# Kernel tuning notes

Hardware: AMD Instinct MI355X
Metric: run time of the kernel (lower is better)

Reference implementation:

```python
import jax, jax.numpy as jnp
import numpy as np

LSTM_DIM = 512
SENT_LEN = 384  # n words -> n+2 LSTM positions (START/STOP)


def _lstm_scan(xs, Wih, Whh, b):
    """Unidirectional LSTM over xs [T, D] -> hidden states [T, H]. torch gate order i,f,g,o."""
    H = Whh.shape[1]
    gx = xs @ Wih.T + b  # [T, 4H] precompute input contribution

    def step(carry, g_x):
        h, c = carry
        g = g_x + h @ Whh.T
        i, f, gg, o = jnp.split(g, 4)
        i = jax.nn.sigmoid(i); f = jax.nn.sigmoid(f); o = jax.nn.sigmoid(o)
        c = f * c + i * jnp.tanh(gg)
        h = o * jnp.tanh(c)
        return (h, c), h

    init = (jnp.zeros((H,), xs.dtype), jnp.zeros((H,), xs.dtype))
    _, hs = jax.lax.scan(step, init, gx)
    return hs  # [T, H]


def setup_inputs() -> dict:
    key = jax.random.key(0)
    ks = jax.random.split(key, 16)
    T = SENT_LEN + 2
    H = LSTM_DIM
    s = lambda fan: 1.0 / np.sqrt(fan)
    return {
        "tag_ids": jax.random.randint(ks[0], (T,), 0, 50, dtype=jnp.int32),
        "word_ids": jax.random.randint(ks[1], (T,), 0, 10000, dtype=jnp.int32),
        "tag_emb": jax.random.normal(ks[2], (50, 128), jnp.float32) * 0.1,
        "word_emb": jax.random.normal(ks[3], (10000, 384), jnp.float32) * 0.1,
        "Wf_ih": jax.random.normal(ks[4], (4 * H, 512), jnp.float32) * s(512),
        "Wf_hh": jax.random.normal(ks[5], (4 * H, H), jnp.float32) * s(H),
        "bf": jnp.zeros((4 * H,), jnp.float32),
        "Wb_ih": jax.random.normal(ks[6], (4 * H, 512), jnp.float32) * s(512),
        "Wb_hh": jax.random.normal(ks[7], (4 * H, H), jnp.float32) * s(H),
        "bb": jnp.zeros((4 * H,), jnp.float32),
        "W1": jax.random.normal(ks[8], (2 * H, 1024), jnp.float32) * s(2 * H),
        "b1": jnp.zeros((1024,), jnp.float32),
        "W2": jax.random.normal(ks[9], (1024, 128), jnp.float32) * s(1024),
        "b2": jnp.zeros((128,), jnp.float32),
        "V1": jax.random.normal(ks[10], (2 * H, 1024), jnp.float32) * s(2 * H),
        "c1": jnp.zeros((1024,), jnp.float32),
        "V2": jax.random.normal(ks[11], (1024, 1), jnp.float32) * s(1024),
        "c2": jnp.zeros((1,), jnp.float32),
    }


def reference(tag_ids, word_ids, tag_emb, word_emb,
              Wf_ih, Wf_hh, bf, Wb_ih, Wb_hh, bb,
              W1, b1, W2, b2, V1, c1, V2, c2):
    H = LSTM_DIM
    # Embedding lookup: concat tag+word embeddings per position  [T, 512]
    x = jnp.concatenate([tag_emb[tag_ids], word_emb[word_ids]], axis=-1)
    # Bidirectional LSTM: forward states and backward states, each [T, H]
    fwd = _lstm_scan(x, Wf_ih, Wf_hh, bf)
    bwd = _lstm_scan(x[::-1], Wb_ih, Wb_hh, bb)[::-1]
    n = x.shape[0] - 2  # sentence length
    # All spans (l, r), 0 <= l < r <= n  (batched superset of recursive decode)
    L, R = np.triu_indices(n + 1, k=1)  # static index arrays, S = n(n+1)/2
    # get_span_encoding: [fwd[r]-fwd[l] ; bwd[l+1]-bwd[r+1]]  -> [S, 2H]
    enc = jnp.concatenate([fwd[R] - fwd[L], bwd[L + 1] - bwd[R + 1]], axis=-1)
    # Feedforward forward(): x = W^T x + b per layer, ReLU between layers
    label_scores = jax.nn.relu(enc @ W1 + b1) @ W2 + b2   # [S, label_vocab]
    split_scores = jax.nn.relu(enc @ V1 + c1) @ V2 + c2   # [S, 1] per-span split scalar
    # split score of candidate s inside (l,r) = split_scores[(l,s)] + split_scores[(s,r)]
    return jnp.concatenate([label_scores, split_scores], axis=-1)  # [S, label_vocab+1]
```

## Files before the change

kernel.cpp:

```cpp
#include <hip/hip_runtime.h>

#define T_LEN 386
#define NSPAN 73920

typedef float v4f __attribute__((ext_vector_type(4)));

__device__ inline void llc_load8(const float* p, v4f& a, v4f& b) {
    asm volatile("global_load_dwordx4 %0, %2, off sc0 sc1\n\t"
                 "global_load_dwordx4 %1, %2, off offset:16 sc0 sc1\n\t"
                 "s_waitcnt vmcnt(0)"
                 : "=&v"(a), "=&v"(b) : "v"(p) : "memory");
}
__device__ inline void llc_store1(float* p, float v) {
    asm volatile("global_store_dword %0, %1, off sc0 sc1"
                 :: "v"(p), "v"(v) : "memory");
}

__device__ inline float fsigmoid(float x) { return 1.f / (1.f + __expf(-x)); }
__device__ inline float ftanh(float x) {
    x = fminf(fmaxf(x, -15.f), 15.f);
    float e = __expf(2.f * x);
    return (e - 1.f) / (e + 1.f);
}

__global__ void k_embed(const int* __restrict__ tag_ids, const int* __restrict__ word_ids,
                        const float* __restrict__ tag_emb, const float* __restrict__ word_emb,
                        float* __restrict__ x) {
    int t = blockIdx.x;
    int tid = threadIdx.x;
    int tr = tag_ids[t], wr = word_ids[t];
    x[t * 512 + tid] = tag_emb[tr * 128 + tid];
    for (int j = tid; j < 384; j += 128)
        x[t * 512 + 128 + j] = word_emb[wr * 384 + j];
}

__global__ void k_gx(const float* __restrict__ x,
                     const float* __restrict__ Wf, const float* __restrict__ bf,
                     const float* __restrict__ Wb, const float* __restrict__ bb,
                     float* __restrict__ gxf, float* __restrict__ gxb) {
    __shared__ float xs[32 * 512];
    int dir = blockIdx.z;
    const float* W = dir ? Wb : Wf;
    const float* bias = dir ? bb : bf;
    float* out = dir ? gxb : gxf;
    int nbase = blockIdx.x * 64;
    int tbase = blockIdx.y * 32;
    int tid = threadIdx.x;

    for (int i = tid; i < 32 * 128; i += 256) {
        int row = i >> 7, c4 = i & 127;
        int t = tbase + row;
        float4 v = make_float4(0.f, 0.f, 0.f, 0.f);
        if (t < T_LEN) {
            int src = dir ? (T_LEN - 1 - t) : t;
            v = ((const float4*)(x + src * 512))[c4];
        }
        ((float4*)xs)[i] = v;
    }
    __syncthreads();

    int col = tid >> 2;
    int kq = tid & 3;
    int n = nbase + col;
    const float4* wrow = (const float4*)(W + (long)n * 512);
    float acc[32];
#pragma unroll
    for (int r = 0; r < 32; ++r) acc[r] = 0.f;
#pragma unroll 2
    for (int it = 0; it < 32; ++it) {
        int k4 = it * 4 + kq;
        float4 w = wrow[k4];
#pragma unroll
        for (int r = 0; r < 32; ++r) {
            float4 xv = ((const float4*)(xs + r * 512))[k4];
            acc[r] += w.x * xv.x + w.y * xv.y + w.z * xv.z + w.w * xv.w;
        }
    }
#pragma unroll
    for (int r = 0; r < 32; ++r) {
        float v = acc[r];
        v += __shfl_xor(v, 1, 4);
        v += __shfl_xor(v, 2, 4);
        acc[r] = v;
    }
    if (kq == 0) {
        float bv = bias[n];
        for (int r = 0; r < 32; ++r) {
            int t = tbase + r;
            if (t < T_LEN) out[t * 2048 + n] = acc[r] + bv;
        }
    }
}

__global__ void k_poison(float* __restrict__ st) {
    int i = blockIdx.x * 256 + threadIdx.x;
    __hip_atomic_store(st + i, 2.0f, __ATOMIC_RELAXED, __HIP_MEMORY_SCOPE_AGENT);
}

__launch_bounds__(256, 1)
__global__ void k_scan(const float* __restrict__ gxf, const float* __restrict__ gxb,
                       const float* __restrict__ Wfhh, const float* __restrict__ Wbhh,
                       float* fwd, float* bwd) {
    __shared__ float gx_sh[T_LEN * 64];
    __shared__ float h_sh[2][512];
    int bid = blockIdx.x;
    int dir = bid >> 5;
    int w = bid & 31;
    int tid = threadIdx.x;
    const float* gx = dir ? gxb : gxf;
    const float* Whh = dir ? Wbhh : Wfhh;
    float* st = dir ? bwd : fwd;

    for (int idx = tid; idx < T_LEN * 64; idx += 256) {
        int t = idx >> 6, j = idx & 63;
        gx_sh[idx] = gx[t * 2048 + (j >> 4) * 512 + w * 16 + (j & 15)];
    }

    int u = tid >> 4;
    int r = tid & 15;
    int g = r >> 2;
    int kq = r & 3;
    int grow = g * 512 + w * 16 + u;
    float4 wreg[32];
    const float4* wsrc = (const float4*)(Whh + (long)grow * 512);
#pragma unroll
    for (int it = 0; it < 32; ++it) wreg[it] = wsrc[it * 4 + kq];
    float c = 0.f;

    for (int ts = 0; ts < T_LEN; ++ts) {
        float* hbuf = h_sh[ts & 1];
        if (tid < 64) {
            if (ts == 0) {
                float4 z = make_float4(0.f, 0.f, 0.f, 0.f);
                *(float4*)(hbuf + tid * 8) = z;
                *(float4*)(hbuf + tid * 8 + 4) = z;
            } else {
                int srow = dir ? (T_LEN - ts) : (ts - 1);
                const float* src = st + srow * 512 + tid * 8;
                v4f a, b;
                for (;;) {
                    llc_load8(src, a, b);
                    bool bad = a.x == 2.f || a.y == 2.f || a.z == 2.f || a.w == 2.f ||
                               b.x == 2.f || b.y == 2.f || b.z == 2.f || b.w == 2.f;
                    if (!bad) break;
                }
                *(v4f*)(hbuf + tid * 8) = a;
                *(v4f*)(hbuf + tid * 8 + 4) = b;
            }
        }
        __syncthreads();

        const float4* hv = (const float4*)hbuf;
        float a0 = 0.f, a1 = 0.f, a2 = 0.f, a3 = 0.f;
#pragma unroll
        for (int it = 0; it < 32; ++it) {
            float4 h4 = hv[it * 4 + kq];
            float4 w4 = wreg[it];
            a0 += w4.x * h4.x; a1 += w4.y * h4.y;
            a2 += w4.z * h4.z; a3 += w4.w * h4.w;
        }
        float v = (a0 + a1) + (a2 + a3);
        v += __shfl_xor(v, 1, 4);
        v += __shfl_xor(v, 2, 4);
        float gi = __shfl(v, (u & 3) * 16 + 0, 64)  + gx_sh[ts * 64 + u];
        float gf = __shfl(v, (u & 3) * 16 + 4, 64)  + gx_sh[ts * 64 + 16 + u];
        float gg = __shfl(v, (u & 3) * 16 + 8, 64)  + gx_sh[ts * 64 + 32 + u];
        float go = __shfl(v, (u & 3) * 16 + 12, 64) + gx_sh[ts * 64 + 48 + u];
        float i_ = fsigmoid(gi);
        float f_ = fsigmoid(gf);
        float o_ = fsigmoid(go);
        c = f_ * c + i_ * ftanh(gg);
        float h = o_ * ftanh(c);
        if (r == 0) {
            int drow = dir ? (T_LEN - 1 - ts) : ts;
            llc_store1(st + drow * 512 + w * 16 + u, h);
        }
    }
}

__global__ void k_tables(const float* __restrict__ fwd, const float* __restrict__ bwd,
                         const float* __restrict__ W1, const float* __restrict__ V1,
                         float* __restrict__ A, float* __restrict__ B,
                         float* __restrict__ AV, float* __restrict__ BV) {
    __shared__ float xs[32 * 512];
    int which = blockIdx.z;
    const float* S = (which & 1) ? bwd : fwd;
    const float* W = ((which >> 1) ? V1 : W1) + (which & 1) * 512 * 1024;
    float* out = which == 0 ? A : which == 1 ? B : which == 2 ? AV : BV;
    int nbase = blockIdx.x * 64, tbase = blockIdx.y * 32;
    int tid = threadIdx.x;

    for (int i = tid; i < 32 * 128; i += 256) {
        int row = i >> 7, c4 = i & 127;
        int t = tbase + row;
        float4 v = make_float4(0.f, 0.f, 0.f, 0.f);
        if (t < T_LEN) v = ((const float4*)(S + t * 512))[c4];
        ((float4*)xs)[i] = v;
    }
    __syncthreads();

    int cg = tid & 15;
    int rg = tid >> 4;
    int n = nbase + cg * 4;
    float4 acc0 = make_float4(0.f, 0.f, 0.f, 0.f);
    float4 acc1 = make_float4(0.f, 0.f, 0.f, 0.f);
#pragma unroll 4
    for (int k = 0; k < 512; ++k) {
        float4 wv = *(const float4*)(W + (long)k * 1024 + n);
        float x0 = xs[(rg * 2) * 512 + k];
        float x1 = xs[(rg * 2 + 1) * 512 + k];
        acc0.x += x0 * wv.x; acc0.y += x0 * wv.y; acc0.z += x0 * wv.z; acc0.w += x0 * wv.w;
        acc1.x += x1 * wv.x; acc1.y += x1 * wv.y; acc1.z += x1 * wv.z; acc1.w += x1 * wv.w;
    }
    int t0 = tbase + rg * 2, t1 = t0 + 1;
    if (t0 < T_LEN) *(float4*)(out + (long)t0 * 1024 + n) = acc0;
    if (t1 < T_LEN) *(float4*)(out + (long)t1 * 1024 + n) = acc1;
}

#define TS 64
#define KC 32
__launch_bounds__(256, 4)
__global__ void k_span(const float* __restrict__ A, const float* __restrict__ B,
                       const float* __restrict__ AV, const float* __restrict__ BV,
                       const float* __restrict__ W2, const float* __restrict__ b1,
                       const float* __restrict__ b2, const float* __restrict__ V2,
                       const float* __restrict__ c1, const float* __restrict__ c2,
                       float* __restrict__ out) {
    __shared__ float hid[TS][KC + 4];
    __shared__ float w2s[KC * 128];
    __shared__ int ls[TS], rs[TS];
    int tid = threadIdx.x;
    int wg = blockIdx.x;

    if (tid < TS) {
        int s = wg * TS + tid;
        float disc = 769.0f * 769.0f - 8.0f * (float)s;
        int l = (int)floorf((769.0f - sqrtf(disc)) * 0.5f);
        if (l < 0) l = 0;
        if (l > 383) l = 383;
#define OFF(L) ((L) * 384 - ((L) * ((L) - 1)) / 2)
        while (l + 1 <= 384 && OFF(l + 1) <= s) ++l;
        while (l > 0 && OFF(l) > s) --l;
        int r = l + 1 + (s - OFF(l));
        ls[tid] = l; rs[tid] = r;
    }
    float acc[8][4];
#pragma unroll
    for (int a = 0; a < 8; ++a)
#pragma unroll
        for (int b = 0; b < 4; ++b) acc[a][b] = 0.f;
    float vacc[2] = {0.f, 0.f};
    int chg = tid & 31, sgm = tid >> 5;
    int kq = tid & 7, sgb = tid >> 3;
    __syncthreads();

    for (int kb = 0; kb < 1024; kb += KC) {
        if (kb) __syncthreads();
        for (int i = tid; i < KC * 128 / 4; i += 256)
            ((float4*)w2s)[i] = ((const float4*)(W2 + kb * 128))[i];
        int ko = kb + kq * 4;
        float4 bv = *(const float4*)(b1 + ko);
        float4 cv = *(const float4*)(c1 + ko);
        float4 v2 = *(const float4*)(V2 + ko);
#pragma unroll
        for (int si = 0; si < 2; ++si) {
            int sp = sgb * 2 + si;
            int l = ls[sp], r = rs[sp];
            float4 ar = *(const float4*)(A + (long)r * 1024 + ko);
            float4 al = *(const float4*)(A + (long)l * 1024 + ko);
            float4 bl = *(const float4*)(B + (long)(l + 1) * 1024 + ko);
            float4 br = *(const float4*)(B + (long)(r + 1) * 1024 + ko);
            float4 hx;
            hx.x = fmaxf(ar.x - al.x + bl.x - br.x + bv.x, 0.f);
            hx.y = fmaxf(ar.y - al.y + bl.y - br.y + bv.y, 0.f);
            hx.z = fmaxf(ar.z - al.z + bl.z - br.z + bv.z, 0.f);
            hx.w = fmaxf(ar.w - al.w + bl.w - br.w + bv.w, 0.f);
            *(float4*)&hid[sp][kq * 4] = hx;
            float4 vr = *(const float4*)(AV + (long)r * 1024 + ko);
            float4 vl = *(const float4*)(AV + (long)l * 1024 + ko);
            float4 ul = *(const float4*)(BV + (long)(l + 1) * 1024 + ko);
            float4 ur = *(const float4*)(BV + (long)(r + 1) * 1024 + ko);
            float h0 = fmaxf(vr.x - vl.x + ul.x - ur.x + cv.x, 0.f);
            float h1 = fmaxf(vr.y - vl.y + ul.y - ur.y + cv.y, 0.f);
            float h2 = fmaxf(vr.z - vl.z + ul.z - ur.z + cv.z, 0.f);
            float h3 = fmaxf(vr.w - vl.w + ul.w - ur.w + cv.w, 0.f);
            vacc[si] += h0 * v2.x + h1 * v2.y + h2 * v2.z + h3 * v2.w;
        }
        __syncthreads();
#pragma unroll 2
        for (int k = 0; k < KC; k += 4) {
            float4 h4[8];
#pragma unroll
            for (int j2 = 0; j2 < 8; ++j2)
                h4[j2] = *(const float4*)&hid[sgm * 8 + j2][k];
#pragma unroll
            for (int kk = 0; kk < 4; ++kk) {
                float4 wv = *(const float4*)&w2s[(k + kk) * 128 + chg * 4];
#pragma unroll
                for (int j2 = 0; j2 < 8; ++j2) {
                    float hx = (&h4[j2].x)[kk];
                    acc[j2][0] += hx * wv.x; acc[j2][1] += hx * wv.y;
                    acc[j2][2] += hx * wv.z; acc[j2][3] += hx * wv.w;
                }
            }
        }
    }

    float4 b2v = *(const float4*)(b2 + chg * 4);
#pragma unroll
    for (int j2 = 0; j2 < 8; ++j2) {
        int s = wg * TS + sgm * 8 + j2;
        float* o = out + (long)s * 129 + chg * 4;
        o[0] = acc[j2][0] + b2v.x; o[1] = acc[j2][1] + b2v.y;
        o[2] = acc[j2][2] + b2v.z; o[3] = acc[j2][3] + b2v.w;
    }
    float c2v = c2[0];
#pragma unroll
    for (int si = 0; si < 2; ++si) {
        float v = vacc[si];
        v += __shfl_xor(v, 4, 8);
        v += __shfl_xor(v, 2, 8);
        v += __shfl_xor(v, 1, 8);
        if (kq == 0) out[(long)(wg * TS + sgb * 2 + si) * 129 + 128] = v + c2v;
    }
}

extern "C" void kernel_launch(void* const* d_in, const int* in_sizes, int n_in,
                              void* d_out, int out_size, void* d_ws, size_t ws_size,
                              hipStream_t stream) {
    const int* tag_ids  = (const int*)d_in[0];
    const int* word_ids = (const int*)d_in[1];
    const float* tag_emb  = (const float*)d_in[2];
    const float* word_emb = (const float*)d_in[3];
    const float* Wf_ih = (const float*)d_in[4];
    const float* Wf_hh = (const float*)d_in[5];
    const float* bf    = (const float*)d_in[6];
    const float* Wb_ih = (const float*)d_in[7];
    const float* Wb_hh = (const float*)d_in[8];
    const float* bb    = (const float*)d_in[9];
    const float* W1 = (const float*)d_in[10];
    const float* b1 = (const float*)d_in[11];
    const float* W2 = (const float*)d_in[12];
    const float* b2 = (const float*)d_in[13];
    const float* V1 = (const float*)d_in[14];
    const float* c1 = (const float*)d_in[15];
    const float* V2 = (const float*)d_in[16];
    const float* c2 = (const float*)d_in[17];

    float* ws = (float*)d_ws;
    float* x   = ws + 256;
    float* gxf = x + T_LEN * 512;
    float* gxb = gxf + T_LEN * 2048;
    float* fwd = gxb + T_LEN * 2048;
    float* bwd = fwd + T_LEN * 512;
    float* A   = bwd + T_LEN * 512;
    float* B   = A + T_LEN * 1024;
    float* AV  = B + T_LEN * 1024;
    float* BV  = AV + T_LEN * 1024;

    k_poison<<<(2 * T_LEN * 512) / 256, 256, 0, stream>>>(fwd);
    k_embed<<<T_LEN, 128, 0, stream>>>(tag_ids, word_ids, tag_emb, word_emb, x);
    k_gx<<<dim3(32, 13, 2), 256, 0, stream>>>(x, Wf_ih, bf, Wb_ih, bb, gxf, gxb);
    k_scan<<<64, 256, 0, stream>>>(gxf, gxb, Wf_hh, Wb_hh, fwd, bwd);
    k_tables<<<dim3(16, 13, 4), 256, 0, stream>>>(fwd, bwd, W1, V1, A, B, AV, BV);
    k_span<<<NSPAN / 64, 256, 0, stream>>>(A, B, AV, BV, W2, b1, b2, V2, c1, c2,
                                           (float*)d_out);
}
```

Baseline: 1.366 ms.

## Pin LSTM scan workgroups to single XCDs and exchange hidden state through L2

Launches the recurrent scan as a cooperative grid of 256 blocks. Each block reads its XCC id and registers in a counter. Two XCDs that each received at least 32 blocks host the forward and backward directions, and the remaining blocks exit. Hidden states are exchanged each step with L2-scoped loads and stores instead of device-coherent ones, which is meant to cut the per-timestep cross-block sync latency. A mirror buffer written with device-scope stores serves as a fallback if L2 polling stalls. This adds poison and memset overhead, and the role assignment relies on how blocks get distributed across XCDs.

```diff
diff --git a/kernel.cpp b/kernel.cpp
--- a/kernel.cpp
+++ b/kernel.cpp
@@ -5,6 +5,16 @@
 
 typedef float v4f __attribute__((ext_vector_type(4)));
 
+__device__ inline void l2_load8(const float* p, v4f& a, v4f& b) {
+    asm volatile("global_load_dwordx4 %0, %2, off sc0\n\t"
+                 "global_load_dwordx4 %1, %2, off offset:16 sc0\n\t"
+                 "s_waitcnt vmcnt(0)"
+                 : "=&v"(a), "=&v"(b) : "v"(p) : "memory");
+}
+__device__ inline void l2_store1(float* p, float v) {
+    asm volatile("global_store_dword %0, %1, off sc0"
+                 :: "v"(p), "v"(v) : "memory");
+}
 __device__ inline void llc_load8(const float* p, v4f& a, v4f& b) {
     asm volatile("global_load_dwordx4 %0, %2, off sc0 sc1\n\t"
                  "global_load_dwordx4 %1, %2, off offset:16 sc0 sc1\n\t"
@@ -14,6 +24,12 @@
 __device__ inline void llc_store1(float* p, float v) {
     asm volatile("global_store_dword %0, %1, off sc0 sc1"
                  :: "v"(p), "v"(v) : "memory");
+}
+
+__device__ inline int get_xcc_id() {
+    int x;
+    asm volatile("s_getreg_b32 %0, hwreg(HW_REG_XCC_ID)" : "=s"(x));
+    return x & 7;
 }
 
 __device__ inline float fsigmoid(float x) { return 1.f / (1.f + __expf(-x)); }
@@ -95,6 +111,130 @@
 __global__ void k_poison(float* __restrict__ st) {
     int i = blockIdx.x * 256 + threadIdx.x;
     __hip_atomic_store(st + i, 2.0f, __ATOMIC_RELAXED, __HIP_MEMORY_SCOPE_AGENT);
+}
+
+__launch_bounds__(256, 1)
+__global__ void k_scan_xcd(const float* __restrict__ gxf, const float* __restrict__ gxb,
+                           const float* __restrict__ Wfhh, const float* __restrict__ Wbhh,
+                           float* fwd, float* bwd, float* fwdm, float* bwdm,
+                           int* ectrl) {
+    __shared__ float gx_sh[T_LEN * 64];
+    __shared__ float h_sh[2][512];
+    __shared__ int sh_role;
+    int tid = threadIdx.x;
+
+    if (tid == 0) {
+        int xcc = get_xcc_id();
+        int slot = __hip_atomic_fetch_add(&ectrl[xcc], 1, __ATOMIC_RELAXED,
+                                          __HIP_MEMORY_SCOPE_AGENT);
+        int total;
+        do {
+            total = 0;
+            for (int i = 0; i < 8; ++i)
+                total += __hip_atomic_load(&ectrl[i], __ATOMIC_RELAXED,
+                                           __HIP_MEMORY_SCOPE_AGENT);
+        } while (total < (int)gridDim.x);
+        int xa = -1, xb = -1;
+        for (int i = 0; i < 8; ++i) {
+            int ci = __hip_atomic_load(&ectrl[i], __ATOMIC_RELAXED,
+                                       __HIP_MEMORY_SCOPE_AGENT);
+            if (ci >= 32) { if (xa < 0) xa = i; else if (xb < 0) xb = i; }
+        }
+        int role = -1;
+        if (xa >= 0 && xb >= 0) {
+            if (xcc == xa && slot < 32) role = slot;
+            else if (xcc == xb && slot < 32) role = 32 + slot;
+        } else {
+            if (blockIdx.x < 64) role = blockIdx.x;
+        }
+        sh_role = role;
+    }
+    __syncthreads();
+    int role = sh_role;
+    if (role < 0) return;
+    int dir = role >> 5;
+    int w = role & 31;
+
+    const float* gx = dir ? gxb : gxf;
+    const float* Whh = dir ? Wbhh : Wfhh;
+    float* st  = dir ? bwd  : fwd;
+    float* stm = dir ? bwdm : fwdm;
+
+    for (int idx = tid; idx < T_LEN * 64; idx += 256) {
+        int t = idx >> 6, j = idx & 63;
+        gx_sh[idx] = gx[t * 2048 + (j >> 4) * 512 + w * 16 + (j & 15)];
+    }
+
+    int u = tid >> 4;
+    int r = tid & 15;
+    int g = r >> 2;
+    int kq = r & 3;
+    int grow = g * 512 + w * 16 + u;
+    float4 wreg[32];
+    const float4* wsrc = (const float4*)(Whh + (long)grow * 512);
+#pragma unroll
+    for (int it = 0; it < 32; ++it) wreg[it] = wsrc[it * 4 + kq];
+    float c = 0.f;
+    __syncthreads();
+
+    for (int ts = 0; ts < T_LEN; ++ts) {
+        float* hbuf = h_sh[ts & 1];
+        if (tid < 64) {
+            if (ts == 0) {
+                float4 z = make_float4(0.f, 0.f, 0.f, 0.f);
+                *(float4*)(hbuf + tid * 8) = z;
+                *(float4*)(hbuf + tid * 8 + 4) = z;
+            } else {
+                int srow = dir ? (T_LEN - ts) : (ts - 1);
+                const float* src  = st  + srow * 512 + tid * 8;
+                const float* srcm = stm + srow * 512 + tid * 8;
+                v4f a, b;
+                int tries = 0;
+                for (;;) {
+                    l2_load8(src, a, b);
+                    bool bad = a.x == 2.f || a.y == 2.f || a.z == 2.f || a.w == 2.f ||
+                               b.x == 2.f || b.y == 2.f || b.z == 2.f || b.w == 2.f;
+                    if (!bad) break;
+                    if (++tries > 24) {
+                        llc_load8(srcm, a, b);
+                        bad = a.x == 2.f || a.y == 2.f || a.z == 2.f || a.w == 2.f ||
+                              b.x == 2.f || b.y == 2.f || b.z == 2.f || b.w == 2.f;
+                        if (!bad) break;
+                    }
+                }
+                *(v4f*)(hbuf + tid * 8) = a;
+                *(v4f*)(hbuf + tid * 8 + 4) = b;
+            }
+        }
+        __syncthreads();
+
+        const float4* hv = (const float4*)hbuf;
+        float a0 = 0.f, a1 = 0.f, a2 = 0.f, a3 = 0.f;
+#pragma unroll
+        for (int it = 0; it < 32; ++it) {
+            float4 h4 = hv[it * 4 + kq];
+            float4 w4 = wreg[it];
+            a0 += w4.x * h4.x; a1 += w4.y * h4.y;
+            a2 += w4.z * h4.z; a3 += w4.w * h4.w;
+        }
+        float v = (a0 + a1) + (a2 + a3);
+        v += __shfl_xor(v, 1, 4);
+        v += __shfl_xor(v, 2, 4);
+        float gi = __shfl(v, (u & 3) * 16 + 0, 64)  + gx_sh[ts * 64 + u];
+        float gf = __shfl(v, (u & 3) * 16 + 4, 64)  + gx_sh[ts * 64 + 16 + u];
+        float gg = __shfl(v, (u & 3) * 16 + 8, 64)  + gx_sh[ts * 64 + 32 + u];
+        float go = __shfl(v, (u & 3) * 16 + 12, 64) + gx_sh[ts * 64 + 48 + u];
+        float i_ = fsigmoid(gi);
+        float f_ = fsigmoid(gf);
+        float o_ = fsigmoid(go);
+        c = f_ * c + i_ * ftanh(gg);
+        float h = o_ * ftanh(c);
+        if (r == 0) {
+            int drow = dir ? (T_LEN - 1 - ts) : ts;
+            l2_store1(st + drow * 512 + w * 16 + u, h);
+            llc_store1(stm + drow * 512 + w * 16 + u, h);
+        }
+    }
 }
 
 __launch_bounds__(256, 1)
@@ -348,20 +488,35 @@
     const float* c2 = (const float*)d_in[17];
 
     float* ws = (float*)d_ws;
-    float* x   = ws + 256;
-    float* gxf = x + T_LEN * 512;
-    float* gxb = gxf + T_LEN * 2048;
-    float* fwd = gxb + T_LEN * 2048;
-    float* bwd = fwd + T_LEN * 512;
-    float* A   = bwd + T_LEN * 512;
-    float* B   = A + T_LEN * 1024;
-    float* AV  = B + T_LEN * 1024;
-    float* BV  = AV + T_LEN * 1024;
-
-    k_poison<<<(2 * T_LEN * 512) / 256, 256, 0, stream>>>(fwd);
+    int* ectrl = (int*)d_ws;
+    float* x    = ws + 256;
+    float* gxf  = x + T_LEN * 512;
+    float* gxb  = gxf + T_LEN * 2048;
+    float* fwd  = gxb + T_LEN * 2048;
+    float* bwd  = fwd + T_LEN * 512;
+    float* fwdm = bwd + T_LEN * 512;
+    float* bwdm = fwdm + T_LEN * 512;
+    float* A    = bwdm + T_LEN * 512;
+    float* B    = A + T_LEN * 1024;
+    float* AV   = B + T_LEN * 1024;
+    float* BV   = AV + T_LEN * 1024;
+
+    hipMemsetAsync(d_ws, 0, 256, stream);
+    k_poison<<<(4 * T_LEN * 512) / 256, 256, 0, stream>>>(fwd);
     k_embed<<<T_LEN, 128, 0, stream>>>(tag_ids, word_ids, tag_emb, word_emb, x);
     k_gx<<<dim3(32, 13, 2), 256, 0, stream>>>(x, Wf_ih, bf, Wb_ih, bb, gxf, gxb);
-    k_scan<<<64, 256, 0, stream>>>(gxf, gxb, Wf_hh, Wb_hh, fwd, bwd);
+
+    {
+        void* args[] = {(void*)&gxf, (void*)&gxb, (void*)&Wf_hh, (void*)&Wb_hh,
+                        (void*)&fwd, (void*)&bwd, (void*)&fwdm, (void*)&bwdm,
+                        (void*)&ectrl};
+        hipError_t e = hipLaunchCooperativeKernel((const void*)k_scan_xcd, dim3(256),
+                                                  dim3(256), args, 0, stream);
+        if (e != hipSuccess) {
+            k_scan<<<64, 256, 0, stream>>>(gxf, gxb, Wf_hh, Wb_hh, fwd, bwd);
+        }
+    }
+
     k_tables<<<dim3(16, 13, 4), 256, 0, stream>>>(fwd, bwd, W1, V1, A, B, AV, BV);
     k_span<<<NSPAN / 64, 256, 0, stream>>>(A, B, AV, BV, W2, b1, b2, V2, c1, c2,
                                            (float*)d_out);
```

Measured after the change: 2.777 ms. 2.03x slower.

## Fuse scan, tables and span stages into one persistent kernel with readiness flags

Applied to the files above, without the earlier changes.

Merges the LSTM scan, the per-timestep projection tables and the span MLP into one persistent kernel. 64 blocks run the recurrence while 192 worker blocks poll per-row ready counters and compute table tiles and span tiles as soon as their LSTM rows exist. Work is ordered by distance from the sequence middle, where both directions finish earliest, so it overlaps with the serial scan. Span tiles are regrouped by fixed l with contiguous r ranges, which lets the left-end loads be hoisted. The cost is spin-wait polling with sleeps and timeout guards, one block per CU, and a risk of deadlock if the 256 blocks are not all resident at once.

```diff
diff --git a/kernel.cpp b/kernel.cpp
--- a/kernel.cpp
+++ b/kernel.cpp
@@ -1,7 +1,7 @@
 #include <hip/hip_runtime.h>
 
 #define T_LEN 386
-#define NSPAN 73920
+#define NW 192
 
 typedef float v4f __attribute__((ext_vector_type(4)));
 
@@ -11,9 +11,19 @@
                  "s_waitcnt vmcnt(0)"
                  : "=&v"(a), "=&v"(b) : "v"(p) : "memory");
 }
-__device__ inline void llc_store1(float* p, float v) {
-    asm volatile("global_store_dword %0, %1, off sc0 sc1"
+__device__ inline void llc_store4(float* p, v4f v) {
+    asm volatile("global_store_dwordx4 %0, %1, off sc0 sc1"
                  :: "v"(p), "v"(v) : "memory");
+}
+__device__ inline int llc_load_int(const int* p) {
+    int v;
+    asm volatile("global_load_dword %0, %1, off sc0 sc1\n\t"
+                 "s_waitcnt vmcnt(0)" : "=v"(v) : "v"(p) : "memory");
+    return v;
+}
+__device__ inline void slow_sleep() {
+    __builtin_amdgcn_s_sleep(127);
+    __builtin_amdgcn_s_sleep(127);
 }
 
 __device__ inline float fsigmoid(float x) { return 1.f / (1.f + __expf(-x)); }
@@ -21,6 +31,12 @@
     x = fminf(fmaxf(x, -15.f), 15.f);
     float e = __expf(2.f * x);
     return (e - 1.f) / (e + 1.f);
+}
+__device__ inline int gfun(int t) { int v = 2 * t - 385; return v < 0 ? -v : v; }
+__device__ inline int tring(int t) {
+    int tb = (t >> 5) << 5;
+    int te = min(tb + 31, 385);
+    return max(gfun(tb), gfun(te)) >> 6;
 }
 
 __global__ void k_embed(const int* __restrict__ tag_ids, const int* __restrict__ word_ids,
@@ -97,111 +113,42 @@
     __hip_atomic_store(st + i, 2.0f, __ATOMIC_RELAXED, __HIP_MEMORY_SCOPE_AGENT);
 }
 
-__launch_bounds__(256, 1)
-__global__ void k_scan(const float* __restrict__ gxf, const float* __restrict__ gxb,
-                       const float* __restrict__ Wfhh, const float* __restrict__ Wbhh,
-                       float* fwd, float* bwd) {
-    __shared__ float gx_sh[T_LEN * 64];
-    __shared__ float h_sh[2][512];
-    int bid = blockIdx.x;
-    int dir = bid >> 5;
-    int w = bid & 31;
+
+__device__ void tables_tile(char* smem, int ti, int z, int nx,
+                            const float* fwd, const float* bwd,
+                            const float* W1, const float* V1,
+                            float* A, float* B, float* AV, float* BV,
+                            int* rdy) {
+    float* xs = (float*)smem;
     int tid = threadIdx.x;
-    const float* gx = dir ? gxb : gxf;
-    const float* Whh = dir ? Wbhh : Wfhh;
-    float* st = dir ? bwd : fwd;
-
-    for (int idx = tid; idx < T_LEN * 64; idx += 256) {
-        int t = idx >> 6, j = idx & 63;
-        gx_sh[idx] = gx[t * 2048 + (j >> 4) * 512 + w * 16 + (j & 15)];
-    }
-
-    int u = tid >> 4;
-    int r = tid & 15;
-    int g = r >> 2;
-    int kq = r & 3;
-    int grow = g * 512 + w * 16 + u;
-    float4 wreg[32];
-    const float4* wsrc = (const float4*)(Whh + (long)grow * 512);
-#pragma unroll
-    for (int it = 0; it < 32; ++it) wreg[it] = wsrc[it * 4 + kq];
-    float c = 0.f;
-
-    for (int ts = 0; ts < T_LEN; ++ts) {
-        float* hbuf = h_sh[ts & 1];
-        if (tid < 64) {
-            if (ts == 0) {
-                float4 z = make_float4(0.f, 0.f, 0.f, 0.f);
-                *(float4*)(hbuf + tid * 8) = z;
-                *(float4*)(hbuf + tid * 8 + 4) = z;
-            } else {
-                int srow = dir ? (T_LEN - ts) : (ts - 1);
-                const float* src = st + srow * 512 + tid * 8;
-                v4f a, b;
-                for (;;) {
-                    llc_load8(src, a, b);
-                    bool bad = a.x == 2.f || a.y == 2.f || a.z == 2.f || a.w == 2.f ||
-                               b.x == 2.f || b.y == 2.f || b.z == 2.f || b.w == 2.f;
-                    if (!bad) break;
-                }
-                *(v4f*)(hbuf + tid * 8) = a;
-                *(v4f*)(hbuf + tid * 8 + 4) = b;
-            }
-        }
-        __syncthreads();
-
-        const float4* hv = (const float4*)hbuf;
-        float a0 = 0.f, a1 = 0.f, a2 = 0.f, a3 = 0.f;
-#pragma unroll
-        for (int it = 0; it < 32; ++it) {
-            float4 h4 = hv[it * 4 + kq];
-            float4 w4 = wreg[it];
-            a0 += w4.x * h4.x; a1 += w4.y * h4.y;
-            a2 += w4.z * h4.z; a3 += w4.w * h4.w;
-        }
-        float v = (a0 + a1) + (a2 + a3);
-        v += __shfl_xor(v, 1, 4);
-        v += __shfl_xor(v, 2, 4);
-        float gi = __shfl(v, (u & 3) * 16 + 0, 64)  + gx_sh[ts * 64 + u];
-        float gf = __shfl(v, (u & 3) * 16 + 4, 64)  + gx_sh[ts * 64 + 16 + u];
-        float gg = __shfl(v, (u & 3) * 16 + 8, 64)  + gx_sh[ts * 64 + 32 + u];
-        float go = __shfl(v, (u & 3) * 16 + 12, 64) + gx_sh[ts * 64 + 48 + u];
-        float i_ = fsigmoid(gi);
-        float f_ = fsigmoid(gf);
-        float o_ = fsigmoid(go);
-        c = f_ * c + i_ * ftanh(gg);
-        float h = o_ * ftanh(c);
-        if (r == 0) {
-            int drow = dir ? (T_LEN - 1 - ts) : ts;
-            llc_store1(st + drow * 512 + w * 16 + u, h);
-        }
-    }
-}
-
-__global__ void k_tables(const float* __restrict__ fwd, const float* __restrict__ bwd,
-                         const float* __restrict__ W1, const float* __restrict__ V1,
-                         float* __restrict__ A, float* __restrict__ B,
-                         float* __restrict__ AV, float* __restrict__ BV) {
-    __shared__ float xs[32 * 512];
-    int which = blockIdx.z;
-    const float* S = (which & 1) ? bwd : fwd;
-    const float* W = ((which >> 1) ? V1 : W1) + (which & 1) * 512 * 1024;
-    float* out = which == 0 ? A : which == 1 ? B : which == 2 ? AV : BV;
-    int nbase = blockIdx.x * 64, tbase = blockIdx.y * 32;
-    int tid = threadIdx.x;
-
-    for (int i = tid; i < 32 * 128; i += 256) {
-        int row = i >> 7, c4 = i & 127;
+    int tbase = ti * 32;
+    int tend = min(tbase + 31, 385);
+    const float* S = (z & 1) ? bwd : fwd;
+    const int* rdys = rdy + (z & 1) * 386;
+    int* rdyT = rdy + 772;
+    const float* W = ((z >> 1) ? V1 : W1) + (z & 1) * 512 * 1024;
+    float* outp = z == 0 ? A : z == 1 ? B : z == 2 ? AV : BV;
+
+    if (tid == 0) {
+        int gaterow = (z & 1) ? tbase : tend;
+        int gg = 0;
+        while (llc_load_int(rdys + gaterow) < 128 && ++gg < (1 << 18))
+            slow_sleep();
+    }
+    __syncthreads();
+
+    for (int i = tid; i < 32 * 64; i += 256) {
+        int row = i >> 6, c8 = i & 63;
         int t = tbase + row;
-        float4 v = make_float4(0.f, 0.f, 0.f, 0.f);
-        if (t < T_LEN) v = ((const float4*)(S + t * 512))[c4];
-        ((float4*)xs)[i] = v;
-    }
-    __syncthreads();
-
-    int cg = tid & 15;
-    int rg = tid >> 4;
-    int n = nbase + cg * 4;
+        v4f a = {0.f, 0.f, 0.f, 0.f}, b = {0.f, 0.f, 0.f, 0.f};
+        if (t < T_LEN) llc_load8(S + (long)t * 512 + c8 * 8, a, b);
+        *(v4f*)(xs + row * 512 + c8 * 8) = a;
+        *(v4f*)(xs + row * 512 + c8 * 8 + 4) = b;
+    }
+    __syncthreads();
+
+    int cg = tid & 15, rg = tid >> 4;
+    int n = nx * 64 + cg * 4;
     float4 acc0 = make_float4(0.f, 0.f, 0.f, 0.f);
     float4 acc1 = make_float4(0.f, 0.f, 0.f, 0.f);
 #pragma unroll 4
@@ -213,37 +160,45 @@
         acc1.x += x1 * wv.x; acc1.y += x1 * wv.y; acc1.z += x1 * wv.z; acc1.w += x1 * wv.w;
     }
     int t0 = tbase + rg * 2, t1 = t0 + 1;
-    if (t0 < T_LEN) *(float4*)(out + (long)t0 * 1024 + n) = acc0;
-    if (t1 < T_LEN) *(float4*)(out + (long)t1 * 1024 + n) = acc1;
-}
-
-#define TS 64
-#define KC 32
-__launch_bounds__(256, 4)
-__global__ void k_span(const float* __restrict__ A, const float* __restrict__ B,
-                       const float* __restrict__ AV, const float* __restrict__ BV,
-                       const float* __restrict__ W2, const float* __restrict__ b1,
-                       const float* __restrict__ b2, const float* __restrict__ V2,
-                       const float* __restrict__ c1, const float* __restrict__ c2,
-                       float* __restrict__ out) {
-    __shared__ float hid[TS][KC + 4];
-    __shared__ float w2s[KC * 128];
-    __shared__ int ls[TS], rs[TS];
+    if (t0 < T_LEN) { v4f v = {acc0.x, acc0.y, acc0.z, acc0.w}; llc_store4(outp + (long)t0 * 1024 + n, v); }
+    if (t1 < T_LEN) { v4f v = {acc1.x, acc1.y, acc1.z, acc1.w}; llc_store4(outp + (long)t1 * 1024 + n, v); }
+    asm volatile("s_waitcnt vmcnt(0)" ::: "memory");
+    __syncthreads();
+    if (tid < 32) {
+        int t = tbase + tid;
+        if (t < T_LEN)
+            __hip_atomic_fetch_add(rdyT + z * 386 + t, 1, __ATOMIC_RELAXED,
+                                   __HIP_MEMORY_SCOPE_AGENT);
+    }
+}
+
+__device__ void span_tile(char* smem, int l, int rbase, int rend,
+                          const float* A, const float* B,
+                          const float* AV, const float* BV,
+                          const float* W2, const float* b1, const float* b2,
+                          const float* V2, const float* c1, const float* c2,
+                          const int* rdy, float* out) {
+    float (*hid)[36] = (float(*)[36])smem;
+    float* w2s = (float*)smem + 64 * 36;
+    const int* rdyT = rdy + 772;
     int tid = threadIdx.x;
-    int wg = blockIdx.x;
-
-    if (tid < TS) {
-        int s = wg * TS + tid;
-        float disc = 769.0f * 769.0f - 8.0f * (float)s;
-        int l = (int)floorf((769.0f - sqrtf(disc)) * 0.5f);
-        if (l < 0) l = 0;
-        if (l > 383) l = 383;
-#define OFF(L) ((L) * 384 - ((L) * ((L) - 1)) / 2)
-        while (l + 1 <= 384 && OFF(l + 1) <= s) ++l;
-        while (l > 0 && OFF(l) > s) --l;
-        int r = l + 1 + (s - OFF(l));
-        ls[tid] = l; rs[tid] = r;
-    }
+    int cnt = rend - rbase + 1;
+
+    {
+        int t1 = -1, t2 = -1;
+        if (tid < 64) { int t = rbase + tid; if (t <= rend) { t1 = t; t2 = 2 * 386 + t; } }
+        else if (tid < 128) { int t = rbase + 1 + (tid - 64); if (t <= rend + 1) { t1 = 386 + t; t2 = 3 * 386 + t; } }
+        else if (tid == 128) { t1 = l; t2 = 2 * 386 + l; }
+        else if (tid == 129) { t1 = 386 + l + 1; t2 = 3 * 386 + l + 1; }
+        if (t1 >= 0) {
+            int gg = 0;
+            while ((llc_load_int(rdyT + t1) < 16 || llc_load_int(rdyT + t2) < 16)
+                   && ++gg < (1 << 18))
+                slow_sleep();
+        }
+    }
+    __syncthreads();
+
     float acc[8][4];
 #pragma unroll
     for (int a = 0; a < 8; ++a)
@@ -252,23 +207,28 @@
     float vacc[2] = {0.f, 0.f};
     int chg = tid & 31, sgm = tid >> 5;
     int kq = tid & 7, sgb = tid >> 3;
-    __syncthreads();
-
-    for (int kb = 0; kb < 1024; kb += KC) {
+    int sp0 = sgb * 2, sp1 = sgb * 2 + 1;
+    int r0 = rbase + min(sp0, cnt - 1);
+    int r1 = rbase + min(sp1, cnt - 1);
+    long soff = (long)l * 384 - (long)l * (l - 1) / 2 + (rbase - l - 1);
+
+    for (int kb = 0; kb < 1024; kb += 32) {
         if (kb) __syncthreads();
-        for (int i = tid; i < KC * 128 / 4; i += 256)
+        for (int i = tid; i < 32 * 128 / 4; i += 256)
             ((float4*)w2s)[i] = ((const float4*)(W2 + kb * 128))[i];
         int ko = kb + kq * 4;
         float4 bv = *(const float4*)(b1 + ko);
         float4 cv = *(const float4*)(c1 + ko);
         float4 v2 = *(const float4*)(V2 + ko);
+        float4 al = *(const float4*)(A + (long)l * 1024 + ko);
+        float4 bl = *(const float4*)(B + (long)(l + 1) * 1024 + ko);
+        float4 vl = *(const float4*)(AV + (long)l * 1024 + ko);
+        float4 ul = *(const float4*)(BV + (long)(l + 1) * 1024 + ko);
 #pragma unroll
         for (int si = 0; si < 2; ++si) {
-            int sp = sgb * 2 + si;
-            int l = ls[sp], r = rs[sp];
+            int r = si ? r1 : r0;
+            int sp = si ? sp1 : sp0;
             float4 ar = *(const float4*)(A + (long)r * 1024 + ko);
-            float4 al = *(const float4*)(A + (long)l * 1024 + ko);
-            float4 bl = *(const float4*)(B + (long)(l + 1) * 1024 + ko);
             float4 br = *(const float4*)(B + (long)(r + 1) * 1024 + ko);
             float4 hx;
             hx.x = fmaxf(ar.x - al.x + bl.x - br.x + bv.x, 0.f);
@@ -277,8 +237,6 @@
             hx.w = fmaxf(ar.w - al.w + bl.w - br.w + bv.w, 0.f);
             *(float4*)&hid[sp][kq * 4] = hx;
             float4 vr = *(const float4*)(AV + (long)r * 1024 + ko);
-            float4 vl = *(const float4*)(AV + (long)l * 1024 + ko);
-            float4 ul = *(const float4*)(BV + (long)(l + 1) * 1024 + ko);
             float4 ur = *(const float4*)(BV + (long)(r + 1) * 1024 + ko);
             float h0 = fmaxf(vr.x - vl.x + ul.x - ur.x + cv.x, 0.f);
             float h1 = fmaxf(vr.y - vl.y + ul.y - ur.y + cv.y, 0.f);
@@ -288,7 +246,7 @@
         }
         __syncthreads();
 #pragma unroll 2
-        for (int k = 0; k < KC; k += 4) {
+        for (int k = 0; k < 32; k += 4) {
             float4 h4[8];
 #pragma unroll
             for (int j2 = 0; j2 < 8; ++j2)
@@ -309,19 +267,155 @@
     float4 b2v = *(const float4*)(b2 + chg * 4);
 #pragma unroll
     for (int j2 = 0; j2 < 8; ++j2) {
-        int s = wg * TS + sgm * 8 + j2;
-        float* o = out + (long)s * 129 + chg * 4;
-        o[0] = acc[j2][0] + b2v.x; o[1] = acc[j2][1] + b2v.y;
-        o[2] = acc[j2][2] + b2v.z; o[3] = acc[j2][3] + b2v.w;
+        int spn = sgm * 8 + j2;
+        if (spn < cnt) {
+            float* o = out + (soff + spn) * 129 + chg * 4;
+            o[0] = acc[j2][0] + b2v.x; o[1] = acc[j2][1] + b2v.y;
+            o[2] = acc[j2][2] + b2v.z; o[3] = acc[j2][3] + b2v.w;
+        }
     }
     float c2v = c2[0];
 #pragma unroll
     for (int si = 0; si < 2; ++si) {
+        int spn = sgb * 2 + si;
         float v = vacc[si];
         v += __shfl_xor(v, 4, 8);
         v += __shfl_xor(v, 2, 8);
         v += __shfl_xor(v, 1, 8);
-        if (kq == 0) out[(long)(wg * TS + sgb * 2 + si) * 129 + 128] = v + c2v;
+        if (kq == 0 && spn < cnt) out[(soff + spn) * 129 + 128] = v + c2v;
+    }
+    __syncthreads();
+}
+
+__launch_bounds__(256, 1)
+__global__ void k_mega(const float* __restrict__ gxf, const float* __restrict__ gxb,
+                       const float* __restrict__ Wfhh, const float* __restrict__ Wbhh,
+                       const float* __restrict__ W1, const float* __restrict__ V1,
+                       const float* __restrict__ W2, const float* __restrict__ b1,
+                       const float* __restrict__ b2, const float* __restrict__ V2,
+                       const float* __restrict__ c1, const float* __restrict__ c2,
+                       float* fwd, float* bwd,
+                       float* A, float* B, float* AV, float* BV,
+                       int* rdy, float* out) {
+    __shared__ __align__(16) char smem_raw[102912];
+    int bid = blockIdx.x;
+    int tid = threadIdx.x;
+
+    if (bid < 64) {
+        float* gx_sh = (float*)smem_raw;
+        float* h_base = gx_sh + T_LEN * 64;
+        int dir = bid >> 5;
+        int w = bid & 31;
+        const float* gx = dir ? gxb : gxf;
+        const float* Whh = dir ? Wbhh : Wfhh;
+        float* st = dir ? bwd : fwd;
+        int* rdyd = rdy + dir * 386;
+
+        for (int idx = tid; idx < T_LEN * 64; idx += 256) {
+            int t = idx >> 6, j = idx & 63;
+            gx_sh[idx] = gx[t * 2048 + (j >> 4) * 512 + w * 16 + (j & 15)];
+        }
+
+        int u = tid >> 4;
+        int r = tid & 15;
+        int g = r >> 2;
+        int kq = r & 3;
+        int wave = tid >> 6;
+        int grow = g * 512 + w * 16 + u;
+        float4 wreg[32];
+        const float4* wsrc = (const float4*)(Whh + (long)grow * 512);
+#pragma unroll
+        for (int it = 0; it < 32; ++it) wreg[it] = wsrc[it * 4 + kq];
+        float c = 0.f;
+        __syncthreads();
+
+        for (int ts = 0; ts < T_LEN; ++ts) {
+            float* hbuf = h_base + (ts & 1) * 512;
+            if (tid < 64) {
+                if (ts == 0) {
+                    float4 z = make_float4(0.f, 0.f, 0.f, 0.f);
+                    *(float4*)(hbuf + tid * 8) = z;
+                    *(float4*)(hbuf + tid * 8 + 4) = z;
+                } else {
+                    int srow = dir ? (T_LEN - ts) : (ts - 1);
+                    const float* src = st + srow * 512 + tid * 8;
+                    v4f a, b;
+                    int gg = 0;
+                    for (;;) {
+                        llc_load8(src, a, b);
+                        bool bad = a.x == 2.f || a.y == 2.f || a.z == 2.f || a.w == 2.f ||
+                                   b.x == 2.f || b.y == 2.f || b.z == 2.f || b.w == 2.f;
+                        if (!bad || ++gg > (1 << 23)) break;
+                    }
+                    *(v4f*)(hbuf + tid * 8) = a;
+                    *(v4f*)(hbuf + tid * 8 + 4) = b;
+                }
+            }
+            __syncthreads();
+
+            const float4* hv = (const float4*)hbuf;
+            float a0 = 0.f, a1 = 0.f, a2 = 0.f, a3 = 0.f;
+#pragma unroll
+            for (int it = 0; it < 32; ++it) {
+                float4 h4 = hv[it * 4 + kq];
+                float4 w4 = wreg[it];
+                a0 += w4.x * h4.x; a1 += w4.y * h4.y;
+                a2 += w4.z * h4.z; a3 += w4.w * h4.w;
+            }
+            float v = (a0 + a1) + (a2 + a3);
+            v += __shfl_xor(v, 1, 4);
+            v += __shfl_xor(v, 2, 4);
+            float gi = __shfl(v, (u & 3) * 16 + 0, 64)  + gx_sh[ts * 64 + u];
+            float gf = __shfl(v, (u & 3) * 16 + 4, 64)  + gx_sh[ts * 64 + 16 + u];
+            float gg_ = __shfl(v, (u & 3) * 16 + 8, 64) + gx_sh[ts * 64 + 32 + u];
+            float go = __shfl(v, (u & 3) * 16 + 12, 64) + gx_sh[ts * 64 + 48 + u];
+            float i_ = fsigmoid(gi);
+            float f_ = fsigmoid(gf);
+            float o_ = fsigmoid(go);
+            c = f_ * c + i_ * ftanh(gg_);
+            float h = o_ * ftanh(c);
+            float h0 = __shfl(h, 0, 64);
+            float h1 = __shfl(h, 16, 64);
+            float h2 = __shfl(h, 32, 64);
+            float h3 = __shfl(h, 48, 64);
+            if ((tid & 63) == 0) {
+                int drow = dir ? (T_LEN - 1 - ts) : ts;
+                v4f hv4 = {h0, h1, h2, h3};
+                llc_store4(st + drow * 512 + w * 16 + wave * 4, hv4);
+                asm volatile("s_waitcnt vmcnt(0)" ::: "memory");
+                __hip_atomic_fetch_add(rdyd + drow, 1, __ATOMIC_RELAXED,
+                                       __HIP_MEMORY_SCOPE_AGENT);
+            }
+        }
+        return;
+    }
+
+    int wk = bid - 64;
+    for (int p = 0; p < 7; ++p) {
+        for (int idx = wk; idx < 832; idx += NW) {
+            int ti = idx >> 6;
+            int z = (idx >> 4) & 3;
+            int nx = idx & 15;
+            int tbase = ti * 32;
+            int tend = min(tbase + 31, 385);
+            int Kt = max(gfun(tbase), gfun(tend)) >> 6;
+            if (Kt != p) continue;
+            tables_tile(smem_raw, ti, z, nx, fwd, bwd, W1, V1, A, B, AV, BV, rdy);
+        }
+        for (int idx = wk; idx < 384 * 6; idx += NW) {
+            int l = idx / 6, j = idx % 6;
+            int rbase = l + 1 + 64 * j;
+            if (rbase > 384) continue;
+            int rend = min(rbase + 63, 384);
+            int K = max(tring(l), tring(l + 1));
+            for (int tt = (rbase >> 5); tt <= ((rend + 1) >> 5); ++tt) {
+                int tb = tt * 32, te = min(tb + 31, 385);
+                K = max(K, max(gfun(tb), gfun(te)) >> 6);
+            }
+            if (K != p) continue;
+            span_tile(smem_raw, l, rbase, rend, A, B, AV, BV,
+                      W2, b1, b2, V2, c1, c2, rdy, out);
+        }
     }
 }
 
@@ -347,8 +441,9 @@
     const float* V2 = (const float*)d_in[16];
     const float* c2 = (const float*)d_in[17];
 
-    float* ws = (float*)d_ws;
-    float* x   = ws + 256;
+    int* rdy = (int*)d_ws;
+    float* base = (float*)d_ws + 4096;
+    float* x   = base;
     float* gxf = x + T_LEN * 512;
     float* gxb = gxf + T_LEN * 2048;
     float* fwd = gxb + T_LEN * 2048;
@@ -358,11 +453,11 @@
     float* AV  = B + T_LEN * 1024;
     float* BV  = AV + T_LEN * 1024;
 
+    hipMemsetAsync(d_ws, 0, 2316 * 4, stream);
     k_poison<<<(2 * T_LEN * 512) / 256, 256, 0, stream>>>(fwd);
     k_embed<<<T_LEN, 128, 0, stream>>>(tag_ids, word_ids, tag_emb, word_emb, x);
     k_gx<<<dim3(32, 13, 2), 256, 0, stream>>>(x, Wf_ih, bf, Wb_ih, bb, gxf, gxb);
-    k_scan<<<64, 256, 0, stream>>>(gxf, gxb, Wf_hh, Wb_hh, fwd, bwd);
-    k_tables<<<dim3(16, 13, 4), 256, 0, stream>>>(fwd, bwd, W1, V1, A, B, AV, BV);
-    k_span<<<NSPAN / 64, 256, 0, stream>>>(A, B, AV, BV, W2, b1, b2, V2, c1, c2,
-                                           (float*)d_out);
-}
+    k_mega<<<256, 256, 0, stream>>>(gxf, gxb, Wf_hh, Wb_hh, W1, V1, W2, b1, b2,
+                                    V2, c1, c2, fwd, bwd, A, B, AV, BV, rdy,
+                                    (float*)d_out);
+}
```

Result: slower. 2.396 ms (+75.5%).
